# Kernel tuning notes

Measured on AMD Instinct MI355X. Metric: run time of the kernel, lower is better.

Reference implementation:

```python
import jax, jax.numpy as jnp
import numpy as np


def setup_inputs() -> dict:
    key = jax.random.key(0)
    ip = jax.random.normal(key, (8, 256, 128, 128), dtype=jnp.float32)
    return {"ip": ip}


def reference(ip):
    b, C, H, W = ip.shape
    two_c = 2 * C
    # precomputed complex shift grid: exp(-1j*2*pi*(C-0.5)*v/(2C)), v = 0..2C-1
    v = jnp.arange(two_c, dtype=jnp.float32)
    angle = -2.0 * jnp.pi * (C - 0.5) * v / two_c
    shift = (jnp.cos(angle) + 1j * jnp.sin(angle)).astype(jnp.complex64)  # [2C]

    viDct = ip * two_c                                   # [b, C, H, W]
    flip_neg = -viDct[:, 1:][:, ::-1]                    # [b, C-1, H, W]
    zeros = jnp.zeros((b, 1, H, W), dtype=ip.dtype)
    rev = jnp.concatenate([viDct, zeros, flip_neg], axis=1)  # [b, 2C, H, W]
    rev = rev.astype(jnp.complex64) * shift[None, :, None, None]
    vxx = jnp.fft.ifft(rev, axis=1)                      # norm='backward' (default)
    out = vxx[:, :C][:, ::-1].real                       # first C, flipped, real part
    return out.astype(ip.dtype)
```

## Files before the change

### kernel.cpp

```cpp
#include <hip/hip_runtime.h>
#include <math.h>

#define NB   8
#define NC   256
#define NHW  (128 * 128)


typedef __attribute__((ext_vector_type(4))) float f32x4;
typedef __attribute__((ext_vector_type(8))) short bf16x8;
typedef __attribute__((ext_vector_type(4))) unsigned int u32x4;

__device__ __forceinline__ unsigned short f2bf(float f) {
    unsigned u = __builtin_bit_cast(unsigned, f);
    u += 0x7fffu + ((u >> 16) & 1u);
    return (unsigned short)(u >> 16);
}

__device__ __forceinline__ unsigned pack2bf(float a, float b) {
    unsigned lo = __builtin_bit_cast(unsigned, a);
    lo += 0x7fffu + ((lo >> 16) & 1u);
    unsigned hi = __builtin_bit_cast(unsigned, b);
    hi += 0x7fffu + ((hi >> 16) & 1u);
    return (lo >> 16) | (hi & 0xffff0000u);
}

__device__ __forceinline__ bf16x8 flip_odd(bf16x8 b) {
    u32x4 u = __builtin_bit_cast(u32x4, b);
    u ^= (u32x4){0x80000000u, 0x80000000u, 0x80000000u, 0x80000000u};
    return __builtin_bit_cast(bf16x8, u);
}

__global__ void coef_kernel(unsigned short* __restrict__ coef) {
    int idx = blockIdx.x * 256 + threadIdx.x;
    int c = idx >> 8;
    int k = idx & 255;
    int t = (k * (2 * c + 1)) & 1023;
    float v = (k == 0) ? 1.0f : 2.0f * cosf((float)t * (float)(M_PI / 512.0));
    coef[idx] = f2bf(v);
}

__global__ __launch_bounds__(256, 4)
void dct_gemm(const float* __restrict__ X, const unsigned short* __restrict__ Mcoef,
              float* __restrict__ Out) {
    const int tid  = threadIdx.x;
    const int lane = tid & 63;
    const int wave = tid >> 6;
    const int m16  = lane & 15;
    const int quad = lane >> 4;

    const int p0 = blockIdx.x * 32;
    const size_t base = (size_t)blockIdx.y * (NC * NHW);
    const float* Xb = X + base + p0;
    float* Ob = Out + base + p0;

    const unsigned short* aP0 = Mcoef + (wave * 32 + m16) * NC + quad * 8;
    const unsigned short* aP1 = aP0 + 16 * NC;

    const float* bP = Xb + (size_t)(quad * 8) * NHW + m16;

    f32x4 acc[2][2][2];
#pragma unroll
    for (int a = 0; a < 2; a++)
#pragma unroll
        for (int b = 0; b < 2; b++)
#pragma unroll
            for (int h = 0; h < 2; h++) acc[a][b][h] = (f32x4){0.f, 0.f, 0.f, 0.f};

#pragma unroll
    for (int kk = 0; kk < 8; kk++) {
        const int kb = kk * 32;

        bf16x8 af0 = *(const bf16x8*)(aP0 + kb);
        bf16x8 af1 = *(const bf16x8*)(aP1 + kb);

        float fb[2][8];
#pragma unroll
        for (int nt = 0; nt < 2; nt++)
#pragma unroll
            for (int j = 0; j < 8; j++)
                fb[nt][j] = bP[(size_t)(kb + j) * NHW + nt * 16];

        bf16x8 bf[2], bn[2];
#pragma unroll
        for (int nt = 0; nt < 2; nt++) {
            u32x4 pk;
#pragma unroll
            for (int j = 0; j < 4; j++)
                pk[j] = pack2bf(fb[nt][2 * j], fb[nt][2 * j + 1]);
            bf[nt] = __builtin_bit_cast(bf16x8, pk);
            bn[nt] = flip_odd(bf[nt]);
        }

        acc[0][0][0] = __builtin_amdgcn_mfma_f32_16x16x32_bf16(af0, bf[0], acc[0][0][0], 0, 0, 0);
        acc[0][1][0] = __builtin_amdgcn_mfma_f32_16x16x32_bf16(af0, bf[1], acc[0][1][0], 0, 0, 0);
        acc[1][0][0] = __builtin_amdgcn_mfma_f32_16x16x32_bf16(af1, bf[0], acc[1][0][0], 0, 0, 0);
        acc[1][1][0] = __builtin_amdgcn_mfma_f32_16x16x32_bf16(af1, bf[1], acc[1][1][0], 0, 0, 0);
        acc[0][0][1] = __builtin_amdgcn_mfma_f32_16x16x32_bf16(af0, bn[0], acc[0][0][1], 0, 0, 0);
        acc[0][1][1] = __builtin_amdgcn_mfma_f32_16x16x32_bf16(af0, bn[1], acc[0][1][1], 0, 0, 0);
        acc[1][0][1] = __builtin_amdgcn_mfma_f32_16x16x32_bf16(af1, bn[0], acc[1][0][1], 0, 0, 0);
        acc[1][1][1] = __builtin_amdgcn_mfma_f32_16x16x32_bf16(af1, bn[1], acc[1][1][1], 0, 0, 0);
    }

#pragma unroll
    for (int mt = 0; mt < 2; mt++) {
        const int cS = wave * 32 + mt * 16 + quad * 4;
#pragma unroll
        for (int nt = 0; nt < 2; nt++) {
            float* o = Ob + nt * 16 + m16;
#pragma unroll
            for (int r = 0; r < 4; r++) {
                o[(size_t)(cS + r) * NHW]       = acc[mt][nt][0][r];
                o[(size_t)(255 - cS - r) * NHW] = acc[mt][nt][1][r];
            }
        }
    }
}

extern "C" void kernel_launch(void* const* d_in, const int* in_sizes, int n_in,
                              void* d_out, int out_size, void* d_ws, size_t ws_size,
                              hipStream_t stream) {
    const float* ip = (const float*)d_in[0];
    float* out = (float*)d_out;
    unsigned short* coef = (unsigned short*)d_ws;

    coef_kernel<<<dim3(128), dim3(256), 0, stream>>>(coef);

    dct_gemm<<<dim3(NHW / 32, NB), dim3(256), 0, stream>>>(ip, coef, out);
}
```

Before: 292.2 us.

## Stage coefficient and input tiles through double-buffered swizzled LDS

Changes the GEMM so that coefficient tiles are loaded straight into LDS with global_load_lds, and input columns are converted to bf16 and written into swizzled LDS buffers. Each of the four K-steps of 64 prefetches the next tile while the MFMAs work on the current one. Each thread now loads one contiguous column strip instead of scattered per-lane reads, which cuts redundant global traffic and hides load latency. In exchange it adds 40KB of LDS per block, which may limit occupancy, plus a barrier on every iteration.

```diff
diff --git a/kernel.cpp b/kernel.cpp
--- a/kernel.cpp
+++ b/kernel.cpp
@@ -5,6 +5,12 @@
 #define NC   256
 #define NHW  (128 * 128)
 
+
+#define BK 64
+#define NITER (NC / BK)
+#define ABUF 16384
+#define XLDS 32768
+#define XBUF 4096
 
 typedef __attribute__((ext_vector_type(4))) float f32x4;
 typedef __attribute__((ext_vector_type(8))) short bf16x8;
@@ -39,9 +45,19 @@
     coef[idx] = f2bf(v);
 }
 
+__device__ __forceinline__ void gload_lds16(const void* g, void* l) {
+    __builtin_amdgcn_global_load_lds(
+        (const __attribute__((address_space(1))) unsigned int*)g,
+        (__attribute__((address_space(3))) unsigned int*)l,
+        16, 0, 0);
+}
+
+
 __global__ __launch_bounds__(256, 4)
 void dct_gemm(const float* __restrict__ X, const unsigned short* __restrict__ Mcoef,
               float* __restrict__ Out) {
+    __shared__ __align__(16) unsigned char lds[40960];
+
     const int tid  = threadIdx.x;
     const int lane = tid & 63;
     const int wave = tid >> 6;
@@ -50,13 +66,18 @@
 
     const int p0 = blockIdx.x * 32;
     const size_t base = (size_t)blockIdx.y * (NC * NHW);
-    const float* Xb = X + base + p0;
+    const float* Xg = X + base;
     float* Ob = Out + base + p0;
 
-    const unsigned short* aP0 = Mcoef + (wave * 32 + m16) * NC + quad * 8;
-    const unsigned short* aP1 = aP0 + 16 * NC;
+    const int aRowT = tid >> 3;
+    const int aSlot = (tid & 7) ^ (aRowT & 7);
+    const unsigned short* aS = Mcoef + aRowT * NC + aSlot * 8;
+    const int aDst = tid * 16;
 
-    const float* bP = Xb + (size_t)(quad * 8) * NHW + m16;
+    const int sp = tid & 31;
+    const int g  = tid >> 5;
+    const float* xS = Xg + (size_t)(g * 8) * NHW + p0 + sp;
+    const int xWoff = sp * 128 + (((g ^ (sp & 7)) & 7) << 4);
 
     f32x4 acc[2][2][2];
 #pragma unroll
@@ -66,39 +87,63 @@
 #pragma unroll
             for (int h = 0; h < 2; h++) acc[a][b][h] = (f32x4){0.f, 0.f, 0.f, 0.f};
 
+    {
+        float v[8];
 #pragma unroll
-    for (int kk = 0; kk < 8; kk++) {
-        const int kb = kk * 32;
+        for (int j = 0; j < 8; j++) v[j] = xS[(size_t)j * NHW];
+#pragma unroll
+        for (int i = 0; i < 4; i++)
+            gload_lds16(aS + i * 32 * NC, lds + i * 4096 + aDst);
+        int4 q = { (int)pack2bf(v[0], v[1]), (int)pack2bf(v[2], v[3]),
+                   (int)pack2bf(v[4], v[5]), (int)pack2bf(v[6], v[7]) };
+        *(int4*)(lds + XLDS + xWoff) = q;
+    }
+    __syncthreads();
 
-        bf16x8 af0 = *(const bf16x8*)(aP0 + kb);
-        bf16x8 af1 = *(const bf16x8*)(aP1 + kb);
+    const int aB = (wave * 32 + m16) * 128;
+    const int xB = m16 * 128;
+    const int rs = m16 & 7;
 
-        float fb[2][8];
+    for (int t = 0; t < NITER; t++) {
+        const int cb = t & 1;
+        const unsigned char* Ac = lds + cb * ABUF;
+        const unsigned char* Xc = lds + XLDS + cb * XBUF;
+
+        float v[8];
+        if (t + 1 < NITER) {
+            const int k1 = (t + 1) * BK;
 #pragma unroll
-        for (int nt = 0; nt < 2; nt++)
+            for (int j = 0; j < 8; j++) v[j] = xS[(size_t)(k1 + j) * NHW];
 #pragma unroll
-            for (int j = 0; j < 8; j++)
-                fb[nt][j] = bP[(size_t)(kb + j) * NHW + nt * 16];
-
-        bf16x8 bf[2], bn[2];
-#pragma unroll
-        for (int nt = 0; nt < 2; nt++) {
-            u32x4 pk;
-#pragma unroll
-            for (int j = 0; j < 4; j++)
-                pk[j] = pack2bf(fb[nt][2 * j], fb[nt][2 * j + 1]);
-            bf[nt] = __builtin_bit_cast(bf16x8, pk);
-            bn[nt] = flip_odd(bf[nt]);
+            for (int i = 0; i < 4; i++)
+                gload_lds16(aS + i * 32 * NC + k1, lds + (cb ^ 1) * ABUF + i * 4096 + aDst);
         }
 
-        acc[0][0][0] = __builtin_amdgcn_mfma_f32_16x16x32_bf16(af0, bf[0], acc[0][0][0], 0, 0, 0);
-        acc[0][1][0] = __builtin_amdgcn_mfma_f32_16x16x32_bf16(af0, bf[1], acc[0][1][0], 0, 0, 0);
-        acc[1][0][0] = __builtin_amdgcn_mfma_f32_16x16x32_bf16(af1, bf[0], acc[1][0][0], 0, 0, 0);
-        acc[1][1][0] = __builtin_amdgcn_mfma_f32_16x16x32_bf16(af1, bf[1], acc[1][1][0], 0, 0, 0);
-        acc[0][0][1] = __builtin_amdgcn_mfma_f32_16x16x32_bf16(af0, bn[0], acc[0][0][1], 0, 0, 0);
-        acc[0][1][1] = __builtin_amdgcn_mfma_f32_16x16x32_bf16(af0, bn[1], acc[0][1][1], 0, 0, 0);
-        acc[1][0][1] = __builtin_amdgcn_mfma_f32_16x16x32_bf16(af1, bn[0], acc[1][0][1], 0, 0, 0);
-        acc[1][1][1] = __builtin_amdgcn_mfma_f32_16x16x32_bf16(af1, bn[1], acc[1][1][1], 0, 0, 0);
+#pragma unroll
+        for (int kk = 0; kk < 2; kk++) {
+            const int so = (((kk * 4 + quad) ^ rs) << 4);
+            bf16x8 af0 = *(const bf16x8*)(Ac + aB + so);
+            bf16x8 af1 = *(const bf16x8*)(Ac + aB + 16 * 128 + so);
+            bf16x8 bf0 = *(const bf16x8*)(Xc + xB + so);
+            bf16x8 bf1 = *(const bf16x8*)(Xc + xB + 16 * 128 + so);
+            bf16x8 bn0 = flip_odd(bf0);
+            bf16x8 bn1 = flip_odd(bf1);
+            acc[0][0][0] = __builtin_amdgcn_mfma_f32_16x16x32_bf16(af0, bf0, acc[0][0][0], 0, 0, 0);
+            acc[0][1][0] = __builtin_amdgcn_mfma_f32_16x16x32_bf16(af0, bf1, acc[0][1][0], 0, 0, 0);
+            acc[1][0][0] = __builtin_amdgcn_mfma_f32_16x16x32_bf16(af1, bf0, acc[1][0][0], 0, 0, 0);
+            acc[1][1][0] = __builtin_amdgcn_mfma_f32_16x16x32_bf16(af1, bf1, acc[1][1][0], 0, 0, 0);
+            acc[0][0][1] = __builtin_amdgcn_mfma_f32_16x16x32_bf16(af0, bn0, acc[0][0][1], 0, 0, 0);
+            acc[0][1][1] = __builtin_amdgcn_mfma_f32_16x16x32_bf16(af0, bn1, acc[0][1][1], 0, 0, 0);
+            acc[1][0][1] = __builtin_amdgcn_mfma_f32_16x16x32_bf16(af1, bn0, acc[1][0][1], 0, 0, 0);
+            acc[1][1][1] = __builtin_amdgcn_mfma_f32_16x16x32_bf16(af1, bn1, acc[1][1][1], 0, 0, 0);
+        }
+
+        if (t + 1 < NITER) {
+            int4 q = { (int)pack2bf(v[0], v[1]), (int)pack2bf(v[2], v[3]),
+                       (int)pack2bf(v[4], v[5]), (int)pack2bf(v[6], v[7]) };
+            *(int4*)(lds + XLDS + (cb ^ 1) * XBUF + xWoff) = q;
+            __syncthreads();
+        }
     }
 
 #pragma unroll
```

Measured after the change: 242.7 us. 16.9% less time.
